# Optimization experiments

Measured on AMD Instinct MI355X. Metric: run time of the kernel, lower is better.

The kernel has to match this reference:

```python
import jax, jax.numpy as jnp
import numpy as np

B, IN, T, E, S, K, W, HD = 4096, 512, 10, 16, 2, 4, 1024, 64


def setup_inputs() -> dict:
    key = jax.random.key(0)
    ks = jax.random.split(key, 12)
    he = lambda k, shp, fan: jax.random.normal(k, shp, jnp.float32) * (2.0 / fan) ** 0.5
    x = jax.random.normal(ks[0], (B, IN + T), jnp.float32)
    return {
        'x': x,
        'gk': he(ks[1], (T, E), T),
        'rk0': he(ks[2], (E, IN, W), IN),
        'rb0': jax.random.normal(ks[3], (E, W), jnp.float32) * 0.01,
        'rk1': he(ks[4], (E, W, W), W),
        'rb1': jax.random.normal(ks[5], (E, W), jnp.float32) * 0.01,
        'sk0': he(ks[6], (S, IN, W), IN),
        'sb0': jax.random.normal(ks[7], (S, W), jnp.float32) * 0.01,
        'sk1': he(ks[8], (S, W, W), W),
        'sb1': jax.random.normal(ks[9], (S, W), jnp.float32) * 0.01,
        'hk': he(ks[10], (T, W, HD), W),
        'hb': jax.random.normal(ks[11], (T, HD), jnp.float32) * 0.01,
    }


def reference(x, gk, rk0, rb0, rk1, rb1, sk0, sb0, sk1, sb1, hk, hb):
    task_idx = x[:, -T:]            # (B, T) task one-hot / features
    feat = x[:, :-T]                # (B, IN)

    # --- top-k routing on task features ---
    gating_logits = task_idx @ gk                       # (B, E)
    topk_idx = jnp.argsort(-gating_logits, axis=-1)[:, :K]  # (B, K)
    topk_logits = jnp.take_along_axis(gating_logits, topk_idx, axis=-1)
    topk_weights = jax.nn.softmax(topk_logits, axis=-1)     # (B, K)

    # --- routed experts: run every expert chain densely, gather at the end ---
    # h: (B, E, d); each expert's independent MLP chain over the same input.
    h = jnp.broadcast_to(feat[:, None, :], (B, E, IN))
    h = jax.nn.relu(jnp.einsum('bei,eij->bej', h, rk0) + rb0[None])  # (B, E, W)
    h = jax.nn.relu(jnp.einsum('bei,eij->bej', h, rk1) + rb1[None])  # (B, E, W)
    h_sel = jnp.take_along_axis(h, topk_idx[:, :, None], axis=1)     # (B, K, W)
    routed = jnp.einsum('bkw,bk->bw', h_sel, topk_weights)           # (B, W)

    # --- shared experts: all run, mean-combined ---
    hs = jnp.broadcast_to(feat[:, None, :], (B, S, IN))
    hs = jax.nn.relu(jnp.einsum('bsi,sij->bsj', hs, sk0) + sb0[None])
    hs = jax.nn.relu(jnp.einsum('bsi,sij->bsj', hs, sk1) + sb1[None])
    shared = hs.mean(axis=1)                                         # (B, W)

    features_out = jnp.tanh(routed + shared)                         # (B, W)

    # --- per-task heads, select by task id ---
    heads_out = jnp.einsum('bw,twd->btd', features_out, hk) + hb[None]  # (B, T, HD)
    task_indices = task_idx.argmax(axis=-1)                             # (B,)
    out = jnp.take_along_axis(heads_out, task_indices[:, None, None], axis=1)[:, 0]
    return out
```

## Files before the change

### kernel.cpp

```cpp
#include <hip/hip_runtime.h>

typedef unsigned short u16;
typedef __attribute__((ext_vector_type(8))) short bf16x8;
typedef __attribute__((ext_vector_type(4))) float f32x4;

constexpr int B_ = 4096, IN_ = 512, T_ = 10, E_ = 16, S_ = 2, K_ = 4, W_ = 1024, HD_ = 64;
constexpr int XROW = IN_ + T_;
constexpr int NPAIR = B_ * (K_ + S_);
constexpr int MTU64 = 400;
constexpr int GEMM_GRID = MTU64 * 8;
constexpr int GB_ = 16;
constexpr int CB_GRID = 1034;


#define GLL16(g, l) __builtin_amdgcn_global_load_lds( \
    (const __attribute__((address_space(1))) void*)(g), \
    (__attribute__((address_space(3))) void*)(l), 16, 0, 0)

__device__ __forceinline__ u16 f2bf(float x) {
    unsigned u = __float_as_uint(x);
    return (u16)((u + 0x7fffu + ((u >> 16) & 1u)) >> 16);
}
__device__ __forceinline__ float bf2f(u16 b) { return __uint_as_float(((unsigned)b) << 16); }

__global__ __launch_bounds__(256) void featconv(const float* __restrict__ x, u16* __restrict__ featb) {
    int i = blockIdx.x * 256 + threadIdx.x;
    int b = i >> 8;
    int c2 = (i & 255) * 2;
    float2 v = *(const float2*)(x + (size_t)b * XROW + c2);
    ushort2 o;
    o.x = f2bf(v.x);
    o.y = f2bf(v.y);
    *(ushort2*)(featb + (size_t)b * IN_ + c2) = o;
}

__global__ __launch_bounds__(256) void gate_kernel(const float* __restrict__ x, const float* __restrict__ gk,
                                                   int* __restrict__ top4p, float* __restrict__ w6,
                                                   int* __restrict__ task_id, int* __restrict__ tpp,
                                                   int* __restrict__ bct_e, int* __restrict__ bct_t) {
    __shared__ float sgk[T_ * E_];
    __shared__ int hist[E_];
    __shared__ int thist[T_];
    int blk = blockIdx.x, tid = threadIdx.x;
    int b = blk * 256 + tid;
    if (tid < T_ * E_) sgk[tid] = gk[tid];
    if (tid < E_) hist[tid] = 0;
    if (tid < T_) thist[tid] = 0;
    __syncthreads();
    float tv[T_];
#pragma unroll
    for (int i = 0; i < T_; ++i) tv[i] = x[(size_t)b * XROW + IN_ + i];
    float lg[E_];
#pragma unroll
    for (int e = 0; e < E_; ++e) {
        float s = 0.f;
#pragma unroll
        for (int i = 0; i < T_; ++i) s += tv[i] * sgk[i * E_ + e];
        lg[e] = s;
    }
    int idx[K_]; float val[K_];
#pragma unroll
    for (int k = 0; k < K_; ++k) {
        int bi = 0; float bv = -1e30f;
#pragma unroll
        for (int e = 0; e < E_; ++e)
            if (lg[e] > bv) { bv = lg[e]; bi = e; }
        idx[k] = bi; val[k] = bv; lg[bi] = -1e30f;
    }
    float m = val[0];
    float ex[K_]; float s = 0.f;
#pragma unroll
    for (int k = 0; k < K_; ++k) { ex[k] = expf(val[k] - m); s += ex[k]; }
    float inv = 1.f / s;
#pragma unroll
    for (int k = 0; k < K_; ++k) {
        int lp = atomicAdd(&hist[idx[k]], 1);
        top4p[b * K_ + k] = idx[k] | (lp << 8);
        w6[b * 6 + k] = ex[k] * inv;
    }
    w6[b * 6 + 4] = 0.5f;
    w6[b * 6 + 5] = 0.5f;
    int ti = 0; float tb = tv[0];
#pragma unroll
    for (int i = 1; i < T_; ++i)
        if (tv[i] > tb) { tb = tv[i]; ti = i; }
    task_id[b] = ti;
    tpp[b] = atomicAdd(&thist[ti], 1);
    __syncthreads();
    if (tid < E_) bct_e[blk * E_ + tid] = hist[tid];
    if (tid < T_) bct_t[blk * T_ + tid] = thist[tid];
}

__global__ void build_tables(const int* __restrict__ bct_e, const int* __restrict__ bct_t,
                             int* __restrict__ meta, int* __restrict__ blockbase,
                             int* __restrict__ tblockbase) {
    __shared__ int cnt_s[E_], tcnt_s[T_], base_s[E_], pb_s[T_];
    int tid = threadIdx.x;
    if (tid < E_) {
        int s = 0;
        for (int blk = 0; blk < GB_; ++blk) s += bct_e[blk * E_ + tid];
        cnt_s[tid] = s;
        meta[tid] = s;
    }
    if (tid >= 32 && tid < 32 + T_) {
        int t = tid - 32;
        int s = 0;
        for (int blk = 0; blk < GB_; ++blk) s += bct_t[blk * T_ + t];
        tcnt_s[t] = s;
        meta[91 + t] = s;
    }
    __syncthreads();
    if (tid == 0) {
        int a = 0;
        for (int e = 0; e < E_; ++e) { base_s[e] = a; meta[16 + e] = a; a += cnt_s[e]; }
        int t = 0;
        for (int g = 0; g < 18; ++g) { meta[48 + g] = t; int c = (g < 16) ? cnt_s[g] : B_; t += (c + 63) >> 6; }
        meta[66] = t;
        int pr = 0, br = 0;
        for (int i = 0; i < T_; ++i) {
            pb_s[i] = pr;
            meta[70 + i] = pr;
            meta[80 + i] = br;
            pr += ((tcnt_s[i] + 3) >> 2) << 2;
            br += (tcnt_s[i] + 3) >> 2;
        }
        meta[90] = br;
    }
    __syncthreads();
    if (tid < E_) {
        int run = base_s[tid];
        for (int blk = 0; blk < GB_; ++blk) { blockbase[blk * E_ + tid] = run; run += bct_e[blk * E_ + tid]; }
    }
    if (tid >= 32 && tid < 32 + T_) {
        int t = tid - 32;
        int run = pb_s[t];
        for (int blk = 0; blk < GB_; ++blk) { tblockbase[blk * T_ + t] = run; run += bct_t[blk * T_ + t]; }
    }
}

__global__ __launch_bounds__(256) void scatter_kernel(const int* __restrict__ top4p,
                                                      const int* __restrict__ blockbase,
                                                      const int* __restrict__ task_id, const int* __restrict__ tpp,
                                                      const int* __restrict__ tblockbase,
                                                      int* __restrict__ pair_sample, int* __restrict__ pair_dst,
                                                      int* __restrict__ torder) {
    int blk = blockIdx.x, tid = threadIdx.x;
    int b = blk * 256 + tid;
#pragma unroll
    for (int k = 0; k < K_; ++k) {
        int v = top4p[b * K_ + k];
        int e = v & 0xFF, lp = v >> 8;
        int p = blockbase[blk * E_ + e] + lp;
        pair_sample[p] = b;
        pair_dst[p] = b * 6 + k;
    }
    pair_sample[B_ * K_ + b] = b;       pair_dst[B_ * K_ + b] = b * 6 + 4;
    pair_sample[B_ * K_ + B_ + b] = b;  pair_dst[B_ * K_ + B_ + b] = b * 6 + 5;
    torder[tblockbase[blk * T_ + task_id[b]] + tpp[b]] = b;
}

__global__ __launch_bounds__(256) void convbf16(const float* __restrict__ in, u16* __restrict__ out) {
    int i = blockIdx.x * 256 + threadIdx.x;
    float4 v = ((const float4*)in)[i];
    ushort4 o;
    o.x = f2bf(v.x); o.y = f2bf(v.y); o.z = f2bf(v.z); o.w = f2bf(v.w);
    ((ushort4*)out)[i] = o;
}

__global__ __launch_bounds__(256) void transconv2(const float* __restrict__ srcA, const float* __restrict__ srcB,
                                                  int splitZ, u16* __restrict__ out, int K, int N) {
    __shared__ float tile[32][33];
    int z = blockIdx.z;
    const float* src = (z < splitZ) ? (srcA + (size_t)z * K * N) : (srcB + (size_t)(z - splitZ) * K * N);
    int k0 = blockIdx.y * 32, n0 = blockIdx.x * 32;
    int tid = threadIdx.x;
    int r = tid >> 3, c4 = (tid & 7) * 4;
    float4 v = *(const float4*)(src + (size_t)(k0 + r) * N + n0 + c4);
    tile[r][c4 + 0] = v.x; tile[r][c4 + 1] = v.y; tile[r][c4 + 2] = v.z; tile[r][c4 + 3] = v.w;
    __syncthreads();
    ushort4 ov;
    ov.x = f2bf(tile[c4 + 0][r]);
    ov.y = f2bf(tile[c4 + 1][r]);
    ov.z = f2bf(tile[c4 + 2][r]);
    ov.w = f2bf(tile[c4 + 3][r]);
    *(ushort4*)(out + (size_t)z * N * K + (size_t)(n0 + r) * K + k0 + c4) = ov;
}

template <int K, int LAYER>
__global__ __launch_bounds__(256, 6) void gemm5(const u16* __restrict__ Asrc, const u16* __restrict__ wT,
                                                const float* __restrict__ rbias, const float* __restrict__ sbias,
                                                const int* __restrict__ pair_sample, const int* __restrict__ pair_dst,
                                                const int* __restrict__ meta, u16* __restrict__ outp) {
    __shared__ char lds[24576];
    const int* tpre = meta + 48;
    const int nwg = tpre[18] * 8;
    int p = blockIdx.x;
    if (p >= nwg) return;
    int q = nwg >> 3, r8 = nwg & 7;
    int xcd = p & 7, iofs = p >> 3;
    int lid = (xcd < r8 ? xcd * (q + 1) : r8 * (q + 1) + (xcd - r8) * q) + iofs;
    int mtu = lid >> 3, nt = lid & 7;
    int e = 0;
    while (mtu >= tpre[e + 1]) ++e;
    int mt = mtu - tpre[e];
    int off, cnt;
    if (e < E_) { off = meta[16 + e]; cnt = meta[e]; }
    else        { off = B_ * K_ + (e - E_) * B_; cnt = B_; }

    const int tid = threadIdx.x;
    const int srow = tid >> 3, sc = tid & 7;
    const u16* wTe = wT + (size_t)e * W_ * K;
    const u16* ab[2];
    const u16* bb[4];
#pragma unroll
    for (int r = 0; r < 2; ++r) {
        int row = r * 32 + srow;
        int swz = (sc ^ (row & 7)) * 8;
        int gm = mt * 64 + row;
        if (gm >= cnt) gm = cnt - 1;
        int arow = (LAYER == 1) ? pair_sample[off + gm] : (off + gm);
        ab[r] = Asrc + (size_t)arow * K + swz;
    }
#pragma unroll
    for (int r = 0; r < 4; ++r) {
        int row = r * 32 + srow;
        int swz = (sc ^ (row & 7)) * 8;
        bb[r] = wTe + (size_t)(nt * 128 + row) * K + swz;
    }

    f32x4 acc[2][4];
#pragma unroll
    for (int i = 0; i < 2; ++i)
#pragma unroll
        for (int j = 0; j < 4; ++j) acc[i][j] = (f32x4){0.f, 0.f, 0.f, 0.f};

    const int lane = tid & 63, wid = tid >> 6;
    const int wr = wid >> 1, wc = wid & 1;
    const int fr = lane & 15;
    const int fkb = (lane >> 4) * 16;

    constexpr int NKT = K / 64;
    for (int kt = 0; kt < NKT; ++kt) {
#pragma unroll
        for (int r = 0; r < 2; ++r) GLL16(ab[r] + kt * 64, lds + r * 4096 + tid * 16);
#pragma unroll
        for (int r = 0; r < 4; ++r) GLL16(bb[r] + kt * 64, lds + 8192 + r * 4096 + tid * 16);
        __syncthreads();
#pragma unroll
        for (int kk = 0; kk < 2; ++kk) {
            bf16x8 af[2], bf[4];
#pragma unroll
            for (int i = 0; i < 2; ++i) {
                int arow = wr * 32 + i * 16 + fr;
                af[i] = *(const bf16x8*)(lds + arow * 128 + ((kk * 64 + fkb) ^ ((arow & 7) << 4)));
            }
#pragma unroll
            for (int j = 0; j < 4; ++j) {
                int brow = wc * 64 + j * 16 + fr;
                bf[j] = *(const bf16x8*)(lds + 8192 + brow * 128 + ((kk * 64 + fkb) ^ ((brow & 7) << 4)));
            }
#pragma unroll
            for (int i = 0; i < 2; ++i)
#pragma unroll
                for (int j = 0; j < 4; ++j)
                    acc[i][j] = __builtin_amdgcn_mfma_f32_16x16x32_bf16(af[i], bf[j], acc[i][j], 0, 0, 0);
        }
        __syncthreads();
    }

    const float* bias = (e < E_) ? (rbias + (size_t)e * W_) : (sbias + (size_t)(e - E_) * W_);
#pragma unroll
    for (int i = 0; i < 2; ++i) {
#pragma unroll
        for (int reg = 0; reg < 4; ++reg) {
            int r = wr * 32 + i * 16 + (lane >> 4) * 4 + reg;
#pragma unroll
            for (int j = 0; j < 4; ++j) {
                int c = wc * 64 + j * 16 + fr;
                float v = acc[i][j][reg] + bias[nt * 128 + c];
                *(u16*)(lds + r * 256 + ((c * 2) ^ ((r & 7) << 4))) = f2bf(fmaxf(v, 0.f));
            }
        }
    }
    __syncthreads();
#pragma unroll
    for (int rr = 0; rr < 4; ++rr) {
        int flat = rr * 4096 + tid * 16;
        int r = flat >> 8;
        int co = flat & 255;
        int m = mt * 64 + r;
        if (m < cnt) {
            int outrow = (LAYER == 1) ? (off + m) : pair_dst[off + m];
            bf16x8 v = *(const bf16x8*)(lds + r * 256 + (co ^ ((r & 7) << 4)));
            *(bf16x8*)(outp + (size_t)outrow * W_ + nt * 128 + (co >> 1)) = v;
        }
    }
}

__global__ __launch_bounds__(256) void combine4(const u16* __restrict__ h2, const float* __restrict__ w6,
                                                const int* __restrict__ torder, const int* __restrict__ meta,
                                                const u16* __restrict__ hkb, const float* __restrict__ hb,
                                                float* __restrict__ out) {
    __shared__ float f[4][W_];
    __shared__ float partials[4][4][64];
    const int* bp = meta + 80;
    int blk = blockIdx.x;
    if (blk >= bp[T_]) return;
    int t = 0;
    while (blk >= bp[t + 1]) ++t;
    int slot0 = meta[70 + t] + (blk - bp[t]) * 4;
    int vend  = meta[70 + t] + meta[91 + t];
    int tid = threadIdx.x;
    int s0 = torder[slot0];
    int smp[4];
#pragma unroll
    for (int i = 0; i < 4; ++i) {
        int v = torder[slot0 + i];
        smp[i] = (slot0 + i < vend) ? v : s0;
    }
#pragma unroll
    for (int s = 0; s < 4; ++s) {
        int b = smp[s];
        float wsl[6];
#pragma unroll
        for (int qq = 0; qq < 6; ++qq) wsl[qq] = w6[b * 6 + qq];
        float sum[4] = {0.f, 0.f, 0.f, 0.f};
#pragma unroll
        for (int qq = 0; qq < 6; ++qq) {
            ushort4 v = *(const ushort4*)(h2 + (size_t)(b * 6 + qq) * W_ + tid * 4);
            sum[0] += wsl[qq] * bf2f(v.x);
            sum[1] += wsl[qq] * bf2f(v.y);
            sum[2] += wsl[qq] * bf2f(v.z);
            sum[3] += wsl[qq] * bf2f(v.w);
        }
#pragma unroll
        for (int i = 0; i < 4; ++i) f[s][tid * 4 + i] = tanhf(sum[i]);
    }
    __syncthreads();
    int d = tid & 63, g = tid >> 6;
    const u16* hp = hkb + (size_t)t * W_ * HD_ + d;
    float acc[4] = {0.f, 0.f, 0.f, 0.f};
#pragma unroll 4
    for (int w = g; w < W_; w += 4) {
        float hv = bf2f(hp[(size_t)w * HD_]);
#pragma unroll
        for (int s = 0; s < 4; ++s) acc[s] += f[s][w] * hv;
    }
#pragma unroll
    for (int s = 0; s < 4; ++s) partials[g][s][d] = acc[s];
    __syncthreads();
    int ss = tid >> 6, dd = tid & 63;
    float r = partials[0][ss][dd] + partials[1][ss][dd] + partials[2][ss][dd] + partials[3][ss][dd]
            + hb[t * HD_ + dd];
    out[(size_t)smp[ss] * HD_ + dd] = r;
}

extern "C" void kernel_launch(void* const* d_in, const int* in_sizes, int n_in,
                              void* d_out, int out_size, void* d_ws, size_t ws_size,
                              hipStream_t stream) {
    const float* x   = (const float*)d_in[0];
    const float* gk  = (const float*)d_in[1];
    const float* rk0 = (const float*)d_in[2];
    const float* rb0 = (const float*)d_in[3];
    const float* rk1 = (const float*)d_in[4];
    const float* rb1 = (const float*)d_in[5];
    const float* sk0 = (const float*)d_in[6];
    const float* sb0 = (const float*)d_in[7];
    const float* sk1 = (const float*)d_in[8];
    const float* sb1 = (const float*)d_in[9];
    const float* hk  = (const float*)d_in[10];
    const float* hb  = (const float*)d_in[11];
    float* out = (float*)d_out;
    (void)in_sizes; (void)n_in; (void)out_size; (void)ws_size;

    char* ws = (char*)d_ws;
    size_t o = 0;
    auto alloc = [&](size_t bytes) { char* p = ws + o; o += (bytes + 255) & ~(size_t)255; return p; };
    int* meta        = (int*)alloc(512);
    int* bct_e       = (int*)alloc((size_t)GB_ * E_ * 4);
    int* bct_t       = (int*)alloc((size_t)GB_ * T_ * 4);
    int* blockbase   = (int*)alloc((size_t)GB_ * E_ * 4);
    int* tblockbase  = (int*)alloc((size_t)GB_ * T_ * 4);
    int* top4p       = (int*)alloc((size_t)B_ * K_ * 4);
    float* w6        = (float*)alloc((size_t)B_ * 6 * 4);
    int* task_id     = (int*)alloc((size_t)B_ * 4);
    int* tpp         = (int*)alloc((size_t)B_ * 4);
    int* pair_sample = (int*)alloc((size_t)NPAIR * 4);
    int* pair_dst    = (int*)alloc((size_t)NPAIR * 4);
    int* torder      = (int*)alloc((size_t)(B_ + 64) * 4);
    u16* featb       = (u16*)alloc((size_t)B_ * IN_ * 2);
    u16* w0T         = (u16*)alloc((size_t)(E_ + S_) * W_ * IN_ * 2);
    u16* w1T         = (u16*)alloc((size_t)(E_ + S_) * W_ * W_ * 2);
    u16* hkb         = (u16*)alloc((size_t)T_ * W_ * HD_ * 2);
    u16* h1          = (u16*)alloc((size_t)NPAIR * W_ * 2);
    u16* h2          = (u16*)alloc((size_t)NPAIR * W_ * 2);

    featconv<<<B_, 256, 0, stream>>>(x, featb);
    gate_kernel<<<GB_, 256, 0, stream>>>(x, gk, top4p, w6, task_id, tpp, bct_e, bct_t);
    build_tables<<<1, 64, 0, stream>>>(bct_e, bct_t, meta, blockbase, tblockbase);
    scatter_kernel<<<GB_, 256, 0, stream>>>(top4p, blockbase, task_id, tpp, tblockbase,
                                            pair_sample, pair_dst, torder);
    transconv2<<<dim3(W_ / 32, IN_ / 32, E_ + S_), 256, 0, stream>>>(rk0, sk0, E_, w0T, IN_, W_);
    transconv2<<<dim3(W_ / 32, W_ / 32, E_ + S_), 256, 0, stream>>>(rk1, sk1, E_, w1T, W_, W_);
    convbf16<<<(T_ * W_ * HD_) / 1024, 256, 0, stream>>>(hk, hkb);
    gemm5<IN_, 1><<<GEMM_GRID, 256, 0, stream>>>(featb, w0T, rb0, sb0, pair_sample, pair_dst, meta, h1);
    gemm5<W_, 2><<<GEMM_GRID, 256, 0, stream>>>(h1, w1T, rb1, sb1, pair_sample, pair_dst, meta, h2);
    combine4<<<CB_GRID, 256, 0, stream>>>(h2, w6, torder, meta, hkb, hb, out);
}
```

Measured before the change: 188.6 us.

## Use 128x128 GEMM tiles with double-buffered LDS prefetch over K-step 32

The grouped expert GEMM moves from 64x128 to 128x128 output tiles, with 4x4 MFMA accumulators per wave. This halves the number of M tiles and raises arithmetic intensity per loaded byte. The K loop now steps by 32 and double-buffers LDS, issuing the next stage's global-to-LDS loads before computing the current stage, with one barrier per iteration instead of two. Expected costs are more registers, lower occupancy (launch bounds drop from 6 to 4), more LDS, and more padding waste on experts whose row counts are not multiples of 128.

```diff
diff --git a/kernel.cpp b/kernel.cpp
--- a/kernel.cpp
+++ b/kernel.cpp
@@ -7,8 +7,8 @@
 constexpr int B_ = 4096, IN_ = 512, T_ = 10, E_ = 16, S_ = 2, K_ = 4, W_ = 1024, HD_ = 64;
 constexpr int XROW = IN_ + T_;
 constexpr int NPAIR = B_ * (K_ + S_);
-constexpr int MTU64 = 400;
-constexpr int GEMM_GRID = MTU64 * 8;
+constexpr int MTU = 208;
+constexpr int GEMM_GRID = MTU * 8;
 constexpr int GB_ = 16;
 constexpr int CB_GRID = 1034;
 
@@ -114,7 +114,7 @@
         int a = 0;
         for (int e = 0; e < E_; ++e) { base_s[e] = a; meta[16 + e] = a; a += cnt_s[e]; }
         int t = 0;
-        for (int g = 0; g < 18; ++g) { meta[48 + g] = t; int c = (g < 16) ? cnt_s[g] : B_; t += (c + 63) >> 6; }
+        for (int g = 0; g < 18; ++g) { meta[48 + g] = t; int c = (g < 16) ? cnt_s[g] : B_; t += (c + 127) >> 7; }
         meta[66] = t;
         int pr = 0, br = 0;
         for (int i = 0; i < T_; ++i) {
@@ -187,11 +187,11 @@
 }
 
 template <int K, int LAYER>
-__global__ __launch_bounds__(256, 6) void gemm5(const u16* __restrict__ Asrc, const u16* __restrict__ wT,
+__global__ __launch_bounds__(256, 4) void gemm6(const u16* __restrict__ Asrc, const u16* __restrict__ wT,
                                                 const float* __restrict__ rbias, const float* __restrict__ sbias,
                                                 const int* __restrict__ pair_sample, const int* __restrict__ pair_dst,
                                                 const int* __restrict__ meta, u16* __restrict__ outp) {
-    __shared__ char lds[24576];
+    __shared__ char lds[32768];
     const int* tpre = meta + 48;
     const int nwg = tpre[18] * 8;
     int p = blockIdx.x;
@@ -208,29 +208,32 @@
     else        { off = B_ * K_ + (e - E_) * B_; cnt = B_; }
 
     const int tid = threadIdx.x;
-    const int srow = tid >> 3, sc = tid & 7;
+    const int srow = tid >> 2, sslot = tid & 3;
     const u16* wTe = wT + (size_t)e * W_ * K;
     const u16* ab[2];
-    const u16* bb[4];
+    const u16* bb[2];
 #pragma unroll
     for (int r = 0; r < 2; ++r) {
-        int row = r * 32 + srow;
-        int swz = (sc ^ (row & 7)) * 8;
-        int gm = mt * 64 + row;
+        int row = r * 64 + srow;
+        int gchunk = sslot ^ ((row >> 1) & 3);
+        int gm = mt * 128 + row;
         if (gm >= cnt) gm = cnt - 1;
         int arow = (LAYER == 1) ? pair_sample[off + gm] : (off + gm);
-        ab[r] = Asrc + (size_t)arow * K + swz;
-    }
-#pragma unroll
-    for (int r = 0; r < 4; ++r) {
-        int row = r * 32 + srow;
-        int swz = (sc ^ (row & 7)) * 8;
-        bb[r] = wTe + (size_t)(nt * 128 + row) * K + swz;
-    }
-
-    f32x4 acc[2][4];
-#pragma unroll
-    for (int i = 0; i < 2; ++i)
+        ab[r] = Asrc + (size_t)arow * K + gchunk * 8;
+        bb[r] = wTe + (size_t)(nt * 128 + row) * K + gchunk * 8;
+    }
+
+    auto STAGE = [&](int kt, int buf) {
+        char* base = lds + buf * 16384;
+        GLL16(ab[0] + kt * 32, base + tid * 16);
+        GLL16(ab[1] + kt * 32, base + 4096 + tid * 16);
+        GLL16(bb[0] + kt * 32, base + 8192 + tid * 16);
+        GLL16(bb[1] + kt * 32, base + 12288 + tid * 16);
+    };
+
+    f32x4 acc[4][4];
+#pragma unroll
+    for (int i = 0; i < 4; ++i)
 #pragma unroll
         for (int j = 0; j < 4; ++j) acc[i][j] = (f32x4){0.f, 0.f, 0.f, 0.f};
 
@@ -239,41 +242,41 @@
     const int fr = lane & 15;
     const int fkb = (lane >> 4) * 16;
 
-    constexpr int NKT = K / 64;
+    constexpr int NKT = K / 32;
+    STAGE(0, 0);
+    asm volatile("s_waitcnt vmcnt(0)" ::: "memory");
+    __builtin_amdgcn_s_barrier();
+    asm volatile("" ::: "memory");
+    int cur = 0;
     for (int kt = 0; kt < NKT; ++kt) {
-#pragma unroll
-        for (int r = 0; r < 2; ++r) GLL16(ab[r] + kt * 64, lds + r * 4096 + tid * 16);
-#pragma unroll
-        for (int r = 0; r < 4; ++r) GLL16(bb[r] + kt * 64, lds + 8192 + r * 4096 + tid * 16);
-        __syncthreads();
-#pragma unroll
-        for (int kk = 0; kk < 2; ++kk) {
-            bf16x8 af[2], bf[4];
-#pragma unroll
-            for (int i = 0; i < 2; ++i) {
-                int arow = wr * 32 + i * 16 + fr;
-                af[i] = *(const bf16x8*)(lds + arow * 128 + ((kk * 64 + fkb) ^ ((arow & 7) << 4)));
-            }
-#pragma unroll
-            for (int j = 0; j < 4; ++j) {
-                int brow = wc * 64 + j * 16 + fr;
-                bf[j] = *(const bf16x8*)(lds + 8192 + brow * 128 + ((kk * 64 + fkb) ^ ((brow & 7) << 4)));
-            }
-#pragma unroll
-            for (int i = 0; i < 2; ++i)
-#pragma unroll
-                for (int j = 0; j < 4; ++j)
-                    acc[i][j] = __builtin_amdgcn_mfma_f32_16x16x32_bf16(af[i], bf[j], acc[i][j], 0, 0, 0);
+        if (kt + 1 < NKT) STAGE(kt + 1, cur ^ 1);
+        char* A = lds + cur * 16384;
+        char* Bv = A + 8192;
+        bf16x8 af[4], bf[4];
+#pragma unroll
+        for (int i = 0; i < 4; ++i) {
+            int arow = wr * 64 + i * 16 + fr;
+            af[i] = *(const bf16x8*)(A + arow * 64 + (fkb ^ (((arow >> 1) & 3) << 4)));
+            int brow = wc * 64 + i * 16 + fr;
+            bf[i] = *(const bf16x8*)(Bv + brow * 64 + (fkb ^ (((brow >> 1) & 3) << 4)));
         }
-        __syncthreads();
+#pragma unroll
+        for (int i = 0; i < 4; ++i)
+#pragma unroll
+            for (int j = 0; j < 4; ++j)
+                acc[i][j] = __builtin_amdgcn_mfma_f32_16x16x32_bf16(af[i], bf[j], acc[i][j], 0, 0, 0);
+        asm volatile("s_waitcnt vmcnt(0)" ::: "memory");
+        __builtin_amdgcn_s_barrier();
+        asm volatile("" ::: "memory");
+        cur ^= 1;
     }
 
     const float* bias = (e < E_) ? (rbias + (size_t)e * W_) : (sbias + (size_t)(e - E_) * W_);
 #pragma unroll
-    for (int i = 0; i < 2; ++i) {
+    for (int i = 0; i < 4; ++i) {
 #pragma unroll
         for (int reg = 0; reg < 4; ++reg) {
-            int r = wr * 32 + i * 16 + (lane >> 4) * 4 + reg;
+            int r = wr * 64 + i * 16 + (lane >> 4) * 4 + reg;
 #pragma unroll
             for (int j = 0; j < 4; ++j) {
                 int c = wc * 64 + j * 16 + fr;
@@ -284,11 +287,11 @@
     }
     __syncthreads();
 #pragma unroll
-    for (int rr = 0; rr < 4; ++rr) {
+    for (int rr = 0; rr < 8; ++rr) {
         int flat = rr * 4096 + tid * 16;
         int r = flat >> 8;
         int co = flat & 255;
-        int m = mt * 64 + r;
+        int m = mt * 128 + r;
         if (m < cnt) {
             int outrow = (LAYER == 1) ? (off + m) : pair_dst[off + m];
             bf16x8 v = *(const bf16x8*)(lds + r * 256 + (co ^ ((r & 7) << 4)));
@@ -403,7 +406,7 @@
     transconv2<<<dim3(W_ / 32, IN_ / 32, E_ + S_), 256, 0, stream>>>(rk0, sk0, E_, w0T, IN_, W_);
     transconv2<<<dim3(W_ / 32, W_ / 32, E_ + S_), 256, 0, stream>>>(rk1, sk1, E_, w1T, W_, W_);
     convbf16<<<(T_ * W_ * HD_) / 1024, 256, 0, stream>>>(hk, hkb);
-    gemm5<IN_, 1><<<GEMM_GRID, 256, 0, stream>>>(featb, w0T, rb0, sb0, pair_sample, pair_dst, meta, h1);
-    gemm5<W_, 2><<<GEMM_GRID, 256, 0, stream>>>(h1, w1T, rb1, sb1, pair_sample, pair_dst, meta, h2);
+    gemm6<IN_, 1><<<GEMM_GRID, 256, 0, stream>>>(featb, w0T, rb0, sb0, pair_sample, pair_dst, meta, h1);
+    gemm6<W_, 2><<<GEMM_GRID, 256, 0, stream>>>(h1, w1T, rb1, sb1, pair_sample, pair_dst, meta, h2);
     combine4<<<CB_GRID, 256, 0, stream>>>(h2, w6, torder, meta, hkb, hb, out);
 }
```

Result: slower. 192.5 us (+2.1%).
